# Kernel optimization log

Hardware: AMD Instinct MI355X
Metric: run time of the kernel (lower is better)

Reference implementation:

```python
import jax, jax.numpy as jnp
import numpy as np

CODEBOOK_SIZE = 8192
CODEBOOK_DIM = 1024
HIDDEN_DIM = 4096
OUT_DIM = 1024
B, M = 32, 576


def setup_inputs() -> dict:
    key = jax.random.key(0)
    k_idx, k_cb, k_w1, k_w2 = jax.random.split(key, 4)
    index = jax.random.randint(k_idx, (B, M), 0, CODEBOOK_SIZE, dtype=jnp.int32)
    # codebook initialized as sqrt(d) * randn, as in the torch module
    codebook = (CODEBOOK_DIM ** 0.5) * jax.random.normal(k_cb, (CODEBOOK_SIZE, CODEBOOK_DIM), dtype=jnp.float32)
    s1 = 1.0 / np.sqrt(CODEBOOK_DIM)
    s2 = 1.0 / np.sqrt(HIDDEN_DIM)
    W1 = s1 * jax.random.normal(k_w1, (CODEBOOK_DIM, HIDDEN_DIM), dtype=jnp.float32)
    b1 = jnp.zeros((HIDDEN_DIM,), dtype=jnp.float32)
    W2 = s2 * jax.random.normal(k_w2, (HIDDEN_DIM, OUT_DIM), dtype=jnp.float32)
    b2 = jnp.zeros((OUT_DIM,), dtype=jnp.float32)
    return {"index": index, "codebook": codebook, "W1": W1, "b1": b1, "W2": W2, "b2": b2}


def reference(index, codebook, W1, b1, W2, b2):
    # one_hot(index) @ codebook is mathematically an index gather:
    # quantized[b, m, :] = codebook[index[b, m], :]
    quantized = jnp.take(codebook, index, axis=0)  # [B, M, D]
    # Decoder_ff: 2-layer GELU MLP (D -> 4D -> D)
    h = jax.nn.gelu(jnp.einsum('bmd,dh->bmh', quantized, W1) + b1)
    rec = jnp.einsum('bmh,ho->bmo', h, W2) + b2
    return rec
```

## Files before the change

### kernel.cpp

```cpp
#include <hip/hip_runtime.h>
#include <stdint.h>

typedef __attribute__((ext_vector_type(8))) short s16x8;
typedef __attribute__((ext_vector_type(4))) float f32x4;

__device__ __forceinline__ short f2bf(float x) {
  uint32_t u = __builtin_bit_cast(uint32_t, x);
  u += 0x7FFFu + ((u >> 16) & 1u);
  return (short)(u >> 16);
}

__device__ __forceinline__ void gload16(void* l, const void* g) {
  __builtin_amdgcn_global_load_lds(
      (const __attribute__((address_space(1))) void*)g,
      (__attribute__((address_space(3))) void*)l, 16, 0, 0);
}

__device__ __forceinline__ float gelu_tanh(float x) {
  float u = 0.7978845608028654f * (x + 0.044715f * x * x * x);
  float e = __expf(2.0f * u);
  return x - x / (e + 1.0f);
}

__global__ void cvt_bf16(const float* __restrict__ in, short* __restrict__ out, int n8) {
  int t = blockIdx.x * 256 + threadIdx.x;
  if (t >= n8) return;
  const float* p = in + (size_t)t * 8;
  s16x8 o;
#pragma unroll
  for (int j = 0; j < 8; ++j) o[j] = f2bf(p[j]);
  *(s16x8*)(out + (size_t)t * 8) = o;
}

__global__ void cvt_T(const float* __restrict__ in, short* __restrict__ out, int K, int N) {
  int Kb = K >> 3;
  int t = blockIdx.x * 256 + threadIdx.x;
  if (t >= N * Kb) return;
  int n = t / Kb;
  int k8 = (t - n * Kb) * 8;
  const float* s = in + (size_t)k8 * N + n;
  s16x8 o;
#pragma unroll
  for (int j = 0; j < 8; ++j) o[j] = f2bf(s[(size_t)j * N]);
  *(s16x8*)(out + (size_t)n * K + k8) = o;
}

template <int MODE, int K, int N>
__global__ __launch_bounds__(512, 2) void gemm8p(
    const short* __restrict__ Asrc, const int* __restrict__ idx,
    const short* __restrict__ Bt, const float* __restrict__ bias,
    void* __restrict__ Cv) {
  __shared__ short lds[65536];

  constexpr int NBN = N / 256;
  const int nwg = gridDim.x;
  int swz = blockIdx.x;
  if ((nwg & 7) == 0) swz = (swz & 7) * (nwg >> 3) + (swz >> 3);
  const int bm = swz / NBN, bn = swz - (swz / NBN) * NBN;

  const int tid = threadIdx.x;
  const int wid = tid >> 6, lane = tid & 63;
  const int wr = wid >> 2, wc = wid & 3;
  const int lr = lane & 15, hi = lane >> 4;

  const int sl = (tid & 7) ^ ((tid >> 3) & 7);
  const short* aptr[4];
  const short* bptr[4];
#pragma unroll
  for (int r = 0; r < 4; ++r) {
    int am = bm * 256 + r * 64 + (tid >> 3);
    long arow = (MODE == 1) ? (long)idx[am] : (long)am;
    aptr[r] = Asrc + arow * (long)K + sl * 8;
    bptr[r] = Bt + (long)(bn * 256 + r * 64 + (tid >> 3)) * K + sl * 8;
  }
  const int wlds = wid * 512;

  const int aRB = (wr * 128 + lr) * 64;
  const int bRB = 16384 + (wc * 64 + lr) * 64;
  const int sk0 = ((0 + hi) ^ (lr & 7)) * 8;
  const int sk1 = ((4 + hi) ^ (lr & 7)) * 8;

  f32x4 acc[8][4] = {};
  s16x8 af[4][2], bf[2][2][2];

  constexpr int NT = K >> 6;

#pragma unroll
  for (int r = 0; r < 4; ++r) gload16(&lds[16384 + r * 4096 + wlds], bptr[r]);
  gload16(&lds[0 * 4096 + wlds], aptr[0]);
  gload16(&lds[2 * 4096 + wlds], aptr[2]);
  gload16(&lds[1 * 4096 + wlds], aptr[1]);
  gload16(&lds[3 * 4096 + wlds], aptr[3]);
  asm volatile("s_waitcnt vmcnt(2)" ::: "memory");
  __builtin_amdgcn_s_barrier();

  for (int t = 0; t < NT; ++t) {
    const int cb = (t & 1) << 15;
    const int nb = cb ^ 32768;
    const int kt = ((t + 1 < NT) ? (t + 1) : 0) << 6;

#pragma unroll
    for (int mi = 0; mi < 4; ++mi) {
      af[mi][0] = *(const s16x8*)&lds[cb + aRB + mi * 1024 + sk0];
      af[mi][1] = *(const s16x8*)&lds[cb + aRB + mi * 1024 + sk1];
    }
#pragma unroll
    for (int ni = 0; ni < 2; ++ni) {
      bf[0][ni][0] = *(const s16x8*)&lds[cb + bRB + ni * 1024 + sk0];
      bf[0][ni][1] = *(const s16x8*)&lds[cb + bRB + ni * 1024 + sk1];
    }
    gload16(&lds[nb + 16384 + 0 * 4096 + wlds], bptr[0] + kt);
    gload16(&lds[nb + 16384 + 1 * 4096 + wlds], bptr[1] + kt);
    __builtin_amdgcn_s_barrier();
    asm volatile("s_waitcnt lgkmcnt(0)" ::: "memory");
    __builtin_amdgcn_s_setprio(1);
#pragma unroll
    for (int mi = 0; mi < 4; ++mi)
#pragma unroll
      for (int ni = 0; ni < 2; ++ni)
#pragma unroll
        for (int ks = 0; ks < 2; ++ks)
          acc[mi][ni] = __builtin_amdgcn_mfma_f32_16x16x32_bf16(af[mi][ks], bf[0][ni][ks], acc[mi][ni], 0, 0, 0);
    __builtin_amdgcn_s_setprio(0);
    __builtin_amdgcn_s_barrier();

#pragma unroll
    for (int ni = 0; ni < 2; ++ni) {
      bf[1][ni][0] = *(const s16x8*)&lds[cb + bRB + 2048 + ni * 1024 + sk0];
      bf[1][ni][1] = *(const s16x8*)&lds[cb + bRB + 2048 + ni * 1024 + sk1];
    }
    gload16(&lds[nb + 16384 + 2 * 4096 + wlds], bptr[2] + kt);
    gload16(&lds[nb + 16384 + 3 * 4096 + wlds], bptr[3] + kt);
    __builtin_amdgcn_s_barrier();
    asm volatile("s_waitcnt lgkmcnt(0)" ::: "memory");
    __builtin_amdgcn_s_setprio(1);
#pragma unroll
    for (int mi = 0; mi < 4; ++mi)
#pragma unroll
      for (int ni = 0; ni < 2; ++ni)
#pragma unroll
        for (int ks = 0; ks < 2; ++ks)
          acc[mi][2 + ni] = __builtin_amdgcn_mfma_f32_16x16x32_bf16(af[mi][ks], bf[1][ni][ks], acc[mi][2 + ni], 0, 0, 0);
    __builtin_amdgcn_s_setprio(0);
    asm volatile("s_waitcnt vmcnt(4)" ::: "memory");
    __builtin_amdgcn_s_barrier();

#pragma unroll
    for (int mi = 0; mi < 4; ++mi) {
      af[mi][0] = *(const s16x8*)&lds[cb + aRB + 4096 + mi * 1024 + sk0];
      af[mi][1] = *(const s16x8*)&lds[cb + aRB + 4096 + mi * 1024 + sk1];
    }
    gload16(&lds[nb + 0 * 4096 + wlds], aptr[0] + kt);
    gload16(&lds[nb + 2 * 4096 + wlds], aptr[2] + kt);
    __builtin_amdgcn_s_barrier();
    asm volatile("s_waitcnt lgkmcnt(0)" ::: "memory");
    __builtin_amdgcn_s_setprio(1);
#pragma unroll
    for (int mi = 0; mi < 4; ++mi)
#pragma unroll
      for (int ni = 0; ni < 2; ++ni)
#pragma unroll
        for (int ks = 0; ks < 2; ++ks)
          acc[4 + mi][ni] = __builtin_amdgcn_mfma_f32_16x16x32_bf16(af[mi][ks], bf[0][ni][ks], acc[4 + mi][ni], 0, 0, 0);
    __builtin_amdgcn_s_setprio(0);
    __builtin_amdgcn_s_barrier();

    gload16(&lds[nb + 1 * 4096 + wlds], aptr[1] + kt);
    gload16(&lds[nb + 3 * 4096 + wlds], aptr[3] + kt);
    __builtin_amdgcn_s_barrier();
    __builtin_amdgcn_s_setprio(1);
#pragma unroll
    for (int mi = 0; mi < 4; ++mi)
#pragma unroll
      for (int ni = 0; ni < 2; ++ni)
#pragma unroll
        for (int ks = 0; ks < 2; ++ks)
          acc[4 + mi][2 + ni] = __builtin_amdgcn_mfma_f32_16x16x32_bf16(af[mi][ks], bf[1][ni][ks], acc[4 + mi][2 + ni], 0, 0, 0);
    __builtin_amdgcn_s_setprio(0);
    asm volatile("s_waitcnt vmcnt(2)" ::: "memory");
    __builtin_amdgcn_s_barrier();
  }

  const int m0 = bm * 256 + wr * 128 + hi * 4;
  const int n0 = bn * 256 + wc * 64 + lr;
#pragma unroll
  for (int j = 0; j < 4; ++j) {
    const int n = n0 + j * 16;
    const float bv = bias[n];
#pragma unroll
    for (int i = 0; i < 8; ++i) {
      f32x4 v = acc[i][j];
#pragma unroll
      for (int r = 0; r < 4; ++r) {
        const int m = m0 + i * 16 + r;
        float x = v[r] + bv;
        if (MODE == 1) {
          ((short*)Cv)[(size_t)m * N + n] = f2bf(gelu_tanh(x));
        } else {
          ((float*)Cv)[(size_t)m * N + n] = x;
        }
      }
    }
  }
}

extern "C" void kernel_launch(void* const* d_in, const int* in_sizes, int n_in,
                              void* d_out, int out_size, void* d_ws, size_t ws_size,
                              hipStream_t stream) {
  const int* idx = (const int*)d_in[0];
  const float* cb = (const float*)d_in[1];
  const float* W1 = (const float*)d_in[2];
  const float* b1 = (const float*)d_in[3];
  const float* W2 = (const float*)d_in[4];
  const float* b2 = (const float*)d_in[5];
  float* out = (float*)d_out;

  char* ws = (char*)d_ws;
  short* cbb = (short*)(ws);
  short* w1t = (short*)(ws + (size_t)16 * 1024 * 1024);
  short* w2t = (short*)(ws + (size_t)24 * 1024 * 1024);
  short* h = (short*)(ws + (size_t)32 * 1024 * 1024);

  cvt_bf16<<<4096, 256, 0, stream>>>(cb, cbb, (8192 * 1024) / 8);
  cvt_T<<<2048, 256, 0, stream>>>(W1, w1t, 1024, 4096);
  cvt_T<<<2048, 256, 0, stream>>>(W2, w2t, 4096, 1024);

  const int Mtot = 32 * 576;
  size_t avail = (ws_size > (size_t)32 * 1024 * 1024) ? ws_size - (size_t)32 * 1024 * 1024 : 0;
  int nc = 1;
  while (nc < 8 && (size_t)(Mtot / nc) * 8192 > avail) nc <<= 1;
  const int Mc = Mtot / nc;

  for (int c = 0; c < nc; ++c) {
    gemm8p<1, 1024, 4096><<<(Mc / 256) * 16, 512, 0, stream>>>(
        cbb, idx + c * Mc, w1t, b1, (void*)h);
    gemm8p<2, 4096, 1024><<<(Mc / 256) * 4, 512, 0, stream>>>(
        h, nullptr, w2t, b2, (void*)(out + (size_t)c * Mc * 1024));
  }
}
```

Measured before the change: 475.5 us.

## Pre-gather codebook rows, use 128-wide N tiles for second GEMM, reorder tile mapping

Replaces the full-codebook bf16 conversion with a gather-and-convert kernel that converts only the 18432 indexed rows into a dense A matrix, so GEMM1 reads contiguous rows instead of indirect ones. The GEMM template gains a BN parameter, and the second GEMM uses 256x128 tiles, doubling its workgroup count from 288 to 576 so more CUs are busy. The tile swizzle now walks M-major within each N column. The costs are a larger workspace footprint and lower arithmetic intensity per GEMM2 tile.

```diff
diff --git a/kernel.cpp b/kernel.cpp
--- a/kernel.cpp
+++ b/kernel.cpp
@@ -22,14 +22,15 @@
   return x - x / (e + 1.0f);
 }
 
-__global__ void cvt_bf16(const float* __restrict__ in, short* __restrict__ out, int n8) {
-  int t = blockIdx.x * 256 + threadIdx.x;
-  if (t >= n8) return;
-  const float* p = in + (size_t)t * 8;
+__global__ void gather_cvt(const float* __restrict__ cb, const int* __restrict__ idx,
+                           short* __restrict__ out) {
+  int m = blockIdx.x * 2 + (threadIdx.x >> 7);
+  int c = (threadIdx.x & 127) * 8;
+  const float* s = cb + (size_t)idx[m] * 1024 + c;
   s16x8 o;
 #pragma unroll
-  for (int j = 0; j < 8; ++j) o[j] = f2bf(p[j]);
-  *(s16x8*)(out + (size_t)t * 8) = o;
+  for (int j = 0; j < 8; ++j) o[j] = f2bf(s[j]);
+  *(s16x8*)(out + (size_t)m * 1024 + c) = o;
 }
 
 __global__ void cvt_T(const float* __restrict__ in, short* __restrict__ out, int K, int N) {
@@ -45,18 +46,22 @@
   *(s16x8*)(out + (size_t)n * K + k8) = o;
 }
 
-template <int MODE, int K, int N>
+template <int MODE, int K, int N, int BN>
 __global__ __launch_bounds__(512, 2) void gemm8p(
-    const short* __restrict__ Asrc, const int* __restrict__ idx,
-    const short* __restrict__ Bt, const float* __restrict__ bias,
-    void* __restrict__ Cv) {
-  __shared__ short lds[65536];
-
-  constexpr int NBN = N / 256;
+    const short* __restrict__ A, const short* __restrict__ Bt,
+    const float* __restrict__ bias, void* __restrict__ Cv) {
+  constexpr int NIH = BN / 128;
+  constexpr int RB = BN / 64;
+  constexpr int ATS = 16384;
+  constexpr int LDSH = (256 + BN) * 64;
+  __shared__ short lds[2 * LDSH];
+
+  constexpr int NBN = N / BN;
   const int nwg = gridDim.x;
+  const int NBM = nwg / NBN;
   int swz = blockIdx.x;
-  if ((nwg & 7) == 0) swz = (swz & 7) * (nwg >> 3) + (swz >> 3);
-  const int bm = swz / NBN, bn = swz - (swz / NBN) * NBN;
+  swz = (swz & 7) * (nwg >> 3) + (swz >> 3);
+  const int bn = swz / NBM, bm = swz - bn * NBM;
 
   const int tid = threadIdx.x;
   const int wid = tid >> 6, lane = tid & 63;
@@ -65,28 +70,27 @@
 
   const int sl = (tid & 7) ^ ((tid >> 3) & 7);
   const short* aptr[4];
-  const short* bptr[4];
-#pragma unroll
-  for (int r = 0; r < 4; ++r) {
-    int am = bm * 256 + r * 64 + (tid >> 3);
-    long arow = (MODE == 1) ? (long)idx[am] : (long)am;
-    aptr[r] = Asrc + arow * (long)K + sl * 8;
-    bptr[r] = Bt + (long)(bn * 256 + r * 64 + (tid >> 3)) * K + sl * 8;
-  }
+  const short* bptr[RB];
+#pragma unroll
+  for (int r = 0; r < 4; ++r)
+    aptr[r] = A + (long)(bm * 256 + r * 64 + (tid >> 3)) * K + sl * 8;
+#pragma unroll
+  for (int r = 0; r < RB; ++r)
+    bptr[r] = Bt + (long)(bn * BN + r * 64 + (tid >> 3)) * K + sl * 8;
   const int wlds = wid * 512;
 
   const int aRB = (wr * 128 + lr) * 64;
-  const int bRB = 16384 + (wc * 64 + lr) * 64;
+  const int bRB = ATS + (wc * (BN / 4) + lr) * 64;
   const int sk0 = ((0 + hi) ^ (lr & 7)) * 8;
   const int sk1 = ((4 + hi) ^ (lr & 7)) * 8;
 
-  f32x4 acc[8][4] = {};
-  s16x8 af[4][2], bf[2][2][2];
+  f32x4 acc[8][2 * NIH] = {};
+  s16x8 af[4][2], bf[2][NIH][2];
 
   constexpr int NT = K >> 6;
 
 #pragma unroll
-  for (int r = 0; r < 4; ++r) gload16(&lds[16384 + r * 4096 + wlds], bptr[r]);
+  for (int r = 0; r < RB; ++r) gload16(&lds[ATS + r * 4096 + wlds], bptr[r]);
   gload16(&lds[0 * 4096 + wlds], aptr[0]);
   gload16(&lds[2 * 4096 + wlds], aptr[2]);
   gload16(&lds[1 * 4096 + wlds], aptr[1]);
@@ -95,8 +99,8 @@
   __builtin_amdgcn_s_barrier();
 
   for (int t = 0; t < NT; ++t) {
-    const int cb = (t & 1) << 15;
-    const int nb = cb ^ 32768;
+    const int cb = (t & 1) * LDSH;
+    const int nb = LDSH - cb;
     const int kt = ((t + 1 < NT) ? (t + 1) : 0) << 6;
 
 #pragma unroll
@@ -105,19 +109,20 @@
       af[mi][1] = *(const s16x8*)&lds[cb + aRB + mi * 1024 + sk1];
     }
 #pragma unroll
-    for (int ni = 0; ni < 2; ++ni) {
+    for (int ni = 0; ni < NIH; ++ni) {
       bf[0][ni][0] = *(const s16x8*)&lds[cb + bRB + ni * 1024 + sk0];
       bf[0][ni][1] = *(const s16x8*)&lds[cb + bRB + ni * 1024 + sk1];
     }
-    gload16(&lds[nb + 16384 + 0 * 4096 + wlds], bptr[0] + kt);
-    gload16(&lds[nb + 16384 + 1 * 4096 + wlds], bptr[1] + kt);
+#pragma unroll
+    for (int r = 0; r < RB / 2; ++r)
+      gload16(&lds[nb + ATS + r * 4096 + wlds], bptr[r] + kt);
     __builtin_amdgcn_s_barrier();
     asm volatile("s_waitcnt lgkmcnt(0)" ::: "memory");
     __builtin_amdgcn_s_setprio(1);
 #pragma unroll
     for (int mi = 0; mi < 4; ++mi)
 #pragma unroll
-      for (int ni = 0; ni < 2; ++ni)
+      for (int ni = 0; ni < NIH; ++ni)
 #pragma unroll
         for (int ks = 0; ks < 2; ++ks)
           acc[mi][ni] = __builtin_amdgcn_mfma_f32_16x16x32_bf16(af[mi][ks], bf[0][ni][ks], acc[mi][ni], 0, 0, 0);
@@ -125,24 +130,26 @@
     __builtin_amdgcn_s_barrier();
 
 #pragma unroll
-    for (int ni = 0; ni < 2; ++ni) {
-      bf[1][ni][0] = *(const s16x8*)&lds[cb + bRB + 2048 + ni * 1024 + sk0];
-      bf[1][ni][1] = *(const s16x8*)&lds[cb + bRB + 2048 + ni * 1024 + sk1];
-    }
-    gload16(&lds[nb + 16384 + 2 * 4096 + wlds], bptr[2] + kt);
-    gload16(&lds[nb + 16384 + 3 * 4096 + wlds], bptr[3] + kt);
+    for (int ni = 0; ni < NIH; ++ni) {
+      bf[1][ni][0] = *(const s16x8*)&lds[cb + bRB + (NIH + ni) * 1024 + sk0];
+      bf[1][ni][1] = *(const s16x8*)&lds[cb + bRB + (NIH + ni) * 1024 + sk1];
+    }
+#pragma unroll
+    for (int r = RB / 2; r < RB; ++r)
+      gload16(&lds[nb + ATS + r * 4096 + wlds], bptr[r] + kt);
     __builtin_amdgcn_s_barrier();
     asm volatile("s_waitcnt lgkmcnt(0)" ::: "memory");
     __builtin_amdgcn_s_setprio(1);
 #pragma unroll
     for (int mi = 0; mi < 4; ++mi)
 #pragma unroll
-      for (int ni = 0; ni < 2; ++ni)
-#pragma unroll
-        for (int ks = 0; ks < 2; ++ks)
-          acc[mi][2 + ni] = __builtin_amdgcn_mfma_f32_16x16x32_bf16(af[mi][ks], bf[1][ni][ks], acc[mi][2 + ni], 0, 0, 0);
-    __builtin_amdgcn_s_setprio(0);
-    asm volatile("s_waitcnt vmcnt(4)" ::: "memory");
+      for (int ni = 0; ni < NIH; ++ni)
+#pragma unroll
+        for (int ks = 0; ks < 2; ++ks)
+          acc[mi][NIH + ni] = __builtin_amdgcn_mfma_f32_16x16x32_bf16(af[mi][ks], bf[1][ni][ks], acc[mi][NIH + ni], 0, 0, 0);
+    __builtin_amdgcn_s_setprio(0);
+    if constexpr (RB == 4) asm volatile("s_waitcnt vmcnt(4)" ::: "memory");
+    else                   asm volatile("s_waitcnt vmcnt(2)" ::: "memory");
     __builtin_amdgcn_s_barrier();
 
 #pragma unroll
@@ -158,7 +165,7 @@
 #pragma unroll
     for (int mi = 0; mi < 4; ++mi)
 #pragma unroll
-      for (int ni = 0; ni < 2; ++ni)
+      for (int ni = 0; ni < NIH; ++ni)
 #pragma unroll
         for (int ks = 0; ks < 2; ++ks)
           acc[4 + mi][ni] = __builtin_amdgcn_mfma_f32_16x16x32_bf16(af[mi][ks], bf[0][ni][ks], acc[4 + mi][ni], 0, 0, 0);
@@ -172,19 +179,19 @@
 #pragma unroll
     for (int mi = 0; mi < 4; ++mi)
 #pragma unroll
-      for (int ni = 0; ni < 2; ++ni)
-#pragma unroll
-        for (int ks = 0; ks < 2; ++ks)
-          acc[4 + mi][2 + ni] = __builtin_amdgcn_mfma_f32_16x16x32_bf16(af[mi][ks], bf[1][ni][ks], acc[4 + mi][2 + ni], 0, 0, 0);
+      for (int ni = 0; ni < NIH; ++ni)
+#pragma unroll
+        for (int ks = 0; ks < 2; ++ks)
+          acc[4 + mi][NIH + ni] = __builtin_amdgcn_mfma_f32_16x16x32_bf16(af[mi][ks], bf[1][ni][ks], acc[4 + mi][NIH + ni], 0, 0, 0);
     __builtin_amdgcn_s_setprio(0);
     asm volatile("s_waitcnt vmcnt(2)" ::: "memory");
     __builtin_amdgcn_s_barrier();
   }
 
   const int m0 = bm * 256 + wr * 128 + hi * 4;
-  const int n0 = bn * 256 + wc * 64 + lr;
-#pragma unroll
-  for (int j = 0; j < 4; ++j) {
+  const int n0 = bn * BN + wc * (BN / 4) + lr;
+#pragma unroll
+  for (int j = 0; j < 2 * NIH; ++j) {
     const int n = n0 + j * 16;
     const float bv = bias[n];
 #pragma unroll
@@ -215,26 +222,27 @@
   const float* b2 = (const float*)d_in[5];
   float* out = (float*)d_out;
 
+  const int Mtot = 32 * 576;
+
   char* ws = (char*)d_ws;
-  short* cbb = (short*)(ws);
-  short* w1t = (short*)(ws + (size_t)16 * 1024 * 1024);
-  short* w2t = (short*)(ws + (size_t)24 * 1024 * 1024);
-  short* h = (short*)(ws + (size_t)32 * 1024 * 1024);
-
-  cvt_bf16<<<4096, 256, 0, stream>>>(cb, cbb, (8192 * 1024) / 8);
+  short* aq = (short*)(ws);
+  short* w1t = (short*)(ws + (size_t)40 * 1024 * 1024);
+  short* w2t = (short*)(ws + (size_t)48 * 1024 * 1024);
+  short* h = (short*)(ws + (size_t)56 * 1024 * 1024);
+
+  gather_cvt<<<Mtot / 2, 256, 0, stream>>>(cb, idx, aq);
   cvt_T<<<2048, 256, 0, stream>>>(W1, w1t, 1024, 4096);
   cvt_T<<<2048, 256, 0, stream>>>(W2, w2t, 4096, 1024);
 
-  const int Mtot = 32 * 576;
-  size_t avail = (ws_size > (size_t)32 * 1024 * 1024) ? ws_size - (size_t)32 * 1024 * 1024 : 0;
+  size_t avail = (ws_size > (size_t)56 * 1024 * 1024) ? ws_size - (size_t)56 * 1024 * 1024 : 0;
   int nc = 1;
   while (nc < 8 && (size_t)(Mtot / nc) * 8192 > avail) nc <<= 1;
   const int Mc = Mtot / nc;
 
   for (int c = 0; c < nc; ++c) {
-    gemm8p<1, 1024, 4096><<<(Mc / 256) * 16, 512, 0, stream>>>(
-        cbb, idx + c * Mc, w1t, b1, (void*)h);
-    gemm8p<2, 4096, 1024><<<(Mc / 256) * 4, 512, 0, stream>>>(
-        h, nullptr, w2t, b2, (void*)(out + (size_t)c * Mc * 1024));
+    gemm8p<1, 1024, 4096, 256><<<(Mc / 256) * 16, 512, 0, stream>>>(
+        aq + (size_t)c * Mc * 1024, w1t, b1, (void*)h);
+    gemm8p<2, 4096, 1024, 128><<<(Mc / 256) * 8, 512, 0, stream>>>(
+        h, w2t, b2, (void*)(out + (size_t)c * Mc * 1024));
   }
 }
```

Result: slower. 514.4 us (+8.2%).
